# Kernel optimization log

Measured on AMD Instinct MI355X. Metric: run time of the kernel, lower is better.

Reference implementation:

```python
import jax, jax.numpy as jnp
import numpy as np

B, C, H, W = 4, 128, 128, 128
_PARAM_IDS = ["1", "2", "4", "5", "7", "8", "9", "10", "12", "13", "15", "16"]


def setup_inputs() -> dict:
    key = jax.random.key(0)
    ks = jax.random.split(key, 2 + 2 * len(_PARAM_IDS))
    scale = 1.0 / np.sqrt(C).astype(np.float32)
    inp = {
        "x": jax.random.normal(ks[0], (B, C, H, W), jnp.float32),
        "y": jax.random.uniform(ks[1], (B, C, H, W), jnp.float32),  # edge gate in [0,1)
    }
    for i, n in enumerate(_PARAM_IDS):
        inp[f"w{n}"] = jax.random.normal(ks[2 + 2 * i], (C, C), jnp.float32) * scale
        inp[f"b{n}"] = jax.random.normal(ks[3 + 2 * i], (C,), jnp.float32) * scale
    return inp


def pw(t, w, b):
    # kernel-size-1 Conv1d: t [B,C,M] -> [B,C,M]
    return jnp.einsum('oc,bcm->bom', w, t) + b[None, :, None]


def gated_scan(seq_x, seq_y, wa, ba, wb, bb, relu_first):
    # seq_x, seq_y: [L, B, C, M]; recurrence h_k = relu(conv_a(x_k) + conv_b(h_{k-1}) * y_{k-1})
    first = jax.nn.relu(seq_x[0]) if relu_first else seq_x[0]

    def step(prev, inp):
        xi, yp = inp
        h = jax.nn.relu(pw(xi, wa, ba) + pw(prev, wb, bb) * yp)
        return h, h

    _, outs = jax.lax.scan(step, first, (seq_x[1:], seq_y[:-1]))
    return jnp.concatenate([first[None], outs], axis=0)


def reference(x, y, w1, b1, w2, b2, w4, b4, w5, b5, w7, b7, w8, b8,
              w9, b9, w10, b10, w12, b12, w13, b13, w15, b15, w16, b16):
    rows_x = jnp.transpose(x, (2, 0, 1, 3))   # [H,B,C,W]
    rows_y = jnp.transpose(y, (2, 0, 1, 3))   # [H,B,C,W]
    y_cols = jnp.transpose(y, (3, 0, 1, 2))   # [W,B,C,H]

    # south scan over height (row 0 untouched, no relu on it)
    hs_rows = gated_scan(rows_x, rows_y, w1, b1, w2, b2, relu_first=False)
    hs_cols = jnp.transpose(hs_rows, (3, 1, 2, 0))  # [W,B,C,H]
    # south-east / south-west scans over width (boundary column gets relu)
    hse = gated_scan(hs_cols, y_cols, w4, b4, w5, b5, relu_first=True)
    hsw = gated_scan(hs_cols[::-1], y_cols[::-1], w7, b7, w8, b8, relu_first=True)[::-1]

    # north scan over height (reversed; boundary row gets relu)
    hn_rows = gated_scan(rows_x[::-1], rows_y[::-1], w9, b9, w10, b10, relu_first=True)[::-1]
    hn_cols = jnp.transpose(hn_rows, (3, 1, 2, 0))  # [W,B,C,H]
    hne = gated_scan(hn_cols, y_cols, w12, b12, w13, b13, relu_first=True)
    hnw = gated_scan(hn_cols[::-1], y_cols[::-1], w15, b15, w16, b16, relu_first=True)[::-1]

    out_cols = hse + hsw + hne + hnw  # [W,B,C,H]
    return jnp.transpose(out_cols, (1, 2, 3, 0))  # [B,C,H,W]
```

## Files before the change

kernel.cpp:

```cpp
#include <hip/hip_runtime.h>

typedef unsigned int uint;
typedef unsigned short ushort;
typedef __attribute__((ext_vector_type(8))) short short8;
typedef __attribute__((ext_vector_type(4))) float f32x4;

#define NPOS 16384
#define PLANE 2097152
#define XR_OFF 0
#define GR_OFF 32768
#define HP_OFF 65536
#define OR_OFF 81920
#define LDS_PH1 81920
#define LDS_PH2 114688

__device__ __forceinline__ uint fbits(float a) { return __builtin_bit_cast(uint, a); }
__device__ __forceinline__ uint rnehi(float a) {
  const uint u = fbits(a);
  return (u + 0x7FFFu + ((u >> 16) & 1u)) & 0xFFFF0000u;
}
__device__ __forceinline__ float fhi(float a) { return __builtin_bit_cast(float, rnehi(a)); }
__device__ __forceinline__ uint packhi(float a, float b) { return (rnehi(a) >> 16) | rnehi(b); }
__device__ __forceinline__ uint packtr(float a, float b) {
  return (fbits(a) >> 16) | (fbits(b) & 0xFFFF0000u);
}
__device__ __forceinline__ float b2f(uint h16) { return __builtin_bit_cast(float, h16 << 16); }

__device__ __forceinline__ f32x4 MF(short8 a, short8 b, f32x4 c) {
  return __builtin_amdgcn_mfma_f32_16x16x32_bf16(a, b, c, 0, 0, 0);
}
__device__ __forceinline__ void fill16(const void* g, char* l) {
  __builtin_amdgcn_global_load_lds((const __attribute__((address_space(1))) void*)g,
                                   (__attribute__((address_space(3))) void*)l, 16, 0, 0);
}
__device__ __forceinline__ void split8(float4 v0, float4 v1, short8& hi, short8& lo) {
  union { short8 s; uint u[4]; } H, L;
  H.u[0] = packhi(v0.x, v0.y); H.u[1] = packhi(v0.z, v0.w);
  H.u[2] = packhi(v1.x, v1.y); H.u[3] = packhi(v1.z, v1.w);
  L.u[0] = packtr(v0.x - fhi(v0.x), v0.y - fhi(v0.y));
  L.u[1] = packtr(v0.z - fhi(v0.z), v0.w - fhi(v0.w));
  L.u[2] = packtr(v1.x - fhi(v1.x), v1.y - fhi(v1.y));
  L.u[3] = packtr(v1.z - fhi(v1.z), v1.w - fhi(v1.w));
  hi = H.s; lo = L.s;
}

#define BAR() asm volatile("s_waitcnt lgkmcnt(0)\n\ts_barrier" ::: "memory")

__global__ __launch_bounds__(256) void k_transpose(const float* __restrict__ x,
                                                   const float* __restrict__ y,
                                                   ushort* __restrict__ xhi,
                                                   ushort* __restrict__ xlo,
                                                   float* __restrict__ yt1,
                                                   float* __restrict__ yt2) {
  __shared__ float tile[128][129];
  const int isY = blockIdx.x >> 9;
  const int id = blockIdx.x & 511;
  const int b = id >> 7, h = id & 127;
  const int t = threadIdx.x, half = t >> 7, lane = t & 127;
  const float* src = (isY ? y : x) + (size_t)b * PLANE + (size_t)h * 128;
  for (int c0 = 0; c0 < 128; c0 += 2) {
    const int c = c0 + half;
    tile[c][lane] = src[(size_t)c * NPOS + lane];
  }
  __syncthreads();
  if (!isY) {
    const int wq = t >> 6, cp = t & 63;
    for (int w0 = 0; w0 < 128; w0 += 4) {
      const int w = w0 + wq;
      const float v0 = tile[2 * cp][w], v1 = tile[2 * cp + 1][w];
      const size_t e = ((size_t)(b * 128 + w) * 128 + h) * 128 + 2 * cp;
      *(uint*)(xhi + e) = packhi(v0, v1);
      *(uint*)(xlo + e) = packtr(v0 - fhi(v0), v1 - fhi(v1));
    }
  } else {
    float* d1 = yt1 + (size_t)b * PLANE + (size_t)h * 128;
    float* d2 = yt2 + ((size_t)(b * 128 + h)) * NPOS;
    for (int w0 = 0; w0 < 128; w0 += 2) {
      const int w = w0 + half;
      const float v = tile[lane][w];
      d1[(size_t)w * NPOS + lane] = v;
      d2[(size_t)w * 128 + lane] = v;
    }
  }
}

template <bool RELU0, bool REV, bool MID, bool OUT16>
__device__ __forceinline__ void scan16(
    char* lds,
    const ushort* __restrict__ xhi, const ushort* __restrict__ xlo, size_t in_base,
    const float* __restrict__ gate, size_t gate_base,
    float* __restrict__ outf, ushort* __restrict__ outhi, ushort* __restrict__ outlo,
    size_t out_base, int out_ps, int out_ls,
    const float* __restrict__ Wa, const float* __restrict__ Ba,
    const float* __restrict__ Wb, const float* __restrict__ Bb,
    int* myflag, int* pflag) {
  const int t = threadIdx.x;
  const int wv = t >> 6, l = t & 63;
  const int line = l & 15, g4 = l >> 4;

  short8 wah[2][4], wal[2][4], wbh[2][4], wbl[2][4];
#pragma unroll
  for (int tt = 0; tt < 2; ++tt)
#pragma unroll
    for (int kt = 0; kt < 4; ++kt) {
      const int row = 32 * wv + 16 * tt + line;
      const int kc = 32 * kt + 8 * g4;
      split8(*(const float4*)(Wa + row * 128 + kc), *(const float4*)(Wa + row * 128 + kc + 4),
             wah[tt][kt], wal[tt][kt]);
      split8(*(const float4*)(Wb + row * 128 + kc), *(const float4*)(Wb + row * 128 + kc + 4),
             wbh[tt][kt], wbl[tt][kt]);
    }
  f32x4 baf[2], bbf[2];
#pragma unroll
  for (int tt = 0; tt < 2; ++tt) {
    baf[tt] = *(const f32x4*)(Ba + 32 * wv + 16 * tt + 4 * g4);
    bbf[tt] = *(const f32x4*)(Bb + 32 * wv + 16 * tt + 4 * g4);
  }

  auto P = [](int p) -> int { return REV ? 127 - p : p; };

  const int sp = wv >> 1;
  const ushort* xsrc = sp ? xlo : xhi;
  const int lf = l & 15;

  auto fillX = [&](int p, int slot) {
#pragma unroll
    for (int f = 0; f < 2; ++f) {
      const int kg = 2 * (wv & 1) + f;
      const int cc = 4 * kg + (l >> 4);
      fill16(xsrc + in_base + (size_t)lf * NPOS + (size_t)p * 128 + 8 * cc,
             lds + XR_OFF + slot * 8192 + sp * 4096 + kg * 1024 + l * 16);
    }
  };
  auto fillG = [&](int p, int slot) {
#pragma unroll
    for (int f = 0; f < 2; ++f)
      fill16(gate + gate_base + (size_t)lf * NPOS + (size_t)p * 128 + 32 * wv + 16 * f + 4 * (l >> 4),
             lds + GR_OFF + slot * 8192 + wv * 2048 + f * 1024 + l * 16);
  };
  auto fillO = [&](int p, int slot) {
#pragma unroll
    for (int f = 0; f < 2; ++f)
      fill16(outf + out_base + (size_t)p * out_ps + (size_t)lf * out_ls + 32 * wv + 16 * f + 4 * (l >> 4),
             lds + OR_OFF + slot * 8192 + wv * 2048 + f * 1024 + l * 16);
  };

#pragma unroll
  for (int p = 0; p < 4; ++p) {
    fillX(P(p), p);
    if (p < 3) fillG(P(p), p);
  }
  asm volatile("s_waitcnt vmcnt(0) lgkmcnt(0)\n\ts_barrier" ::: "memory");

  {
    char* Hwr = lds + HP_OFF;
#pragma unroll
    for (int tt = 0; tt < 2; ++tt) {
      const int cw = 4 * wv + 2 * tt + (g4 >> 1);
      const int boff = (cw * 16 + line) * 16 + 8 * (g4 & 1);
      const uint2 xh = *(const uint2*)(lds + XR_OFF + boff);
      const uint2 xl = *(const uint2*)(lds + XR_OFF + 4096 + boff);
      float4 f;
      f.x = b2f(xh.x & 0xFFFFu) + b2f(xl.x & 0xFFFFu);
      f.y = b2f(xh.x >> 16) + b2f(xl.x >> 16);
      f.z = b2f(xh.y & 0xFFFFu) + b2f(xl.y & 0xFFFFu);
      f.w = b2f(xh.y >> 16) + b2f(xl.y >> 16);
      if (RELU0) {
        f.x = fmaxf(f.x, 0.f); f.y = fmaxf(f.y, 0.f);
        f.z = fmaxf(f.z, 0.f); f.w = fmaxf(f.w, 0.f);
      }
      uint2 hw, lw;
      hw.x = packhi(f.x, f.y); hw.y = packhi(f.z, f.w);
      lw.x = packtr(f.x - fhi(f.x), f.y - fhi(f.y));
      lw.y = packtr(f.z - fhi(f.z), f.w - fhi(f.w));
      *(uint2*)(Hwr + boff) = hw;
      *(uint2*)(Hwr + 4096 + boff) = lw;
      const int ci0 = 32 * wv + 16 * tt + 4 * g4;
      const size_t oe = out_base + (size_t)P(0) * out_ps + (size_t)line * out_ls + ci0;
      if (OUT16) {
        *(uint2*)(outhi + oe) = hw;
        *(uint2*)(outlo + oe) = lw;
      } else {
        *(float4*)(outf + oe) = f;
      }
    }
  }
  BAR();

#pragma unroll 1
  for (int s = 1; s < 128; ++s) {
    if (MID && s == 64) {
      while (__hip_atomic_load(pflag, __ATOMIC_RELAXED, __HIP_MEMORY_SCOPE_AGENT) == 0)
        __builtin_amdgcn_s_sleep(1);
      fillO(P(64), 0);
      fillO(P(65), 1);
      fillO(P(66), 2);
    }
    if (s <= 124) {
      fillX(P(s + 3), (s + 3) & 3);
      fillG(P(s + 2), (s + 2) & 3);
      if (MID && s >= 64) fillO(P(s + 3), (s + 3) & 3);
    }
    if (MID && s == 64)
      asm volatile("s_waitcnt vmcnt(10)" ::: "memory");

    const f32x4 z = {0.f, 0.f, 0.f, 0.f};
    f32x4 aF0 = baf[0], aF1 = baf[1], aR0 = bbf[0], aR1 = bbf[1];
    f32x4 cF0 = z, cF1 = z, cR0 = z, cR1 = z;
    const char* H = lds + HP_OFF + ((s - 1) & 1) * 8192;
    const char* X = lds + XR_OFF + (s & 3) * 8192;
    __builtin_amdgcn_s_setprio(1);
#define KT(kt, F0, F1, R0, R1)                                            \
    {                                                                     \
      const short8 hh = *(const short8*)(H + kt * 1024 + l * 16);         \
      const short8 hl = *(const short8*)(H + 4096 + kt * 1024 + l * 16);  \
      const short8 xh = *(const short8*)(X + kt * 1024 + l * 16);         \
      const short8 xl = *(const short8*)(X + 4096 + kt * 1024 + l * 16);  \
      R0 = MF(wbh[0][kt], hh, R0);                                        \
      R1 = MF(wbh[1][kt], hh, R1);                                        \
      F0 = MF(wah[0][kt], xh, F0);                                        \
      F1 = MF(wah[1][kt], xh, F1);                                        \
      R0 = MF(wbh[0][kt], hl, R0);                                        \
      R1 = MF(wbh[1][kt], hl, R1);                                        \
      F0 = MF(wah[0][kt], xl, F0);                                        \
      F1 = MF(wah[1][kt], xl, F1);                                        \
      R0 = MF(wbl[0][kt], hh, R0);                                        \
      R1 = MF(wbl[1][kt], hh, R1);                                        \
      F0 = MF(wal[0][kt], xh, F0);                                        \
      F1 = MF(wal[1][kt], xh, F1);                                        \
    }
    KT(0, aF0, aF1, aR0, aR1)
    KT(1, cF0, cF1, cR0, cR1)
    KT(2, aF0, aF1, aR0, aR1)
    KT(3, cF0, cF1, cR0, cR1)
#undef KT
    __builtin_amdgcn_s_setprio(0);
    aF0 += cF0; aF1 += cF1; aR0 += cR0; aR1 += cR1;

    const char* Grd = lds + GR_OFF + ((s - 1) & 3) * 8192 + wv * 2048;
    const char* Ord = lds + OR_OFF + (s & 3) * 8192 + wv * 2048;
    char* Hwr = lds + HP_OFF + (s & 1) * 8192;
    const f32x4 aR[2] = {aR0, aR1}, aF[2] = {aF0, aF1};
#pragma unroll
    for (int tt = 0; tt < 2; ++tt) {
      const f32x4 g = *(const f32x4*)(Grd + tt * 1024 + l * 16);
      float4 h;
      h.x = fmaxf(fmaf(aR[tt][0], g[0], aF[tt][0]), 0.f);
      h.y = fmaxf(fmaf(aR[tt][1], g[1], aF[tt][1]), 0.f);
      h.z = fmaxf(fmaf(aR[tt][2], g[2], aF[tt][2]), 0.f);
      h.w = fmaxf(fmaf(aR[tt][3], g[3], aF[tt][3]), 0.f);
      uint2 hw, lw;
      hw.x = packhi(h.x, h.y); hw.y = packhi(h.z, h.w);
      lw.x = packtr(h.x - fhi(h.x), h.y - fhi(h.y));
      lw.y = packtr(h.z - fhi(h.z), h.w - fhi(h.w));
      const int cw = 4 * wv + 2 * tt + (g4 >> 1);
      const int boff = (cw * 16 + line) * 16 + 8 * (g4 & 1);
      *(uint2*)(Hwr + boff) = hw;
      *(uint2*)(Hwr + 4096 + boff) = lw;
      const int ci0 = 32 * wv + 16 * tt + 4 * g4;
      const size_t oe = out_base + (size_t)P(s) * out_ps + (size_t)line * out_ls + ci0;
      if (OUT16) {
        *(uint2*)(outhi + oe) = hw;
        *(uint2*)(outlo + oe) = lw;
      } else {
        float4 o = h;
        if (MID && s >= 64) {
          const f32x4 ov = *(const f32x4*)(Ord + tt * 1024 + l * 16);
          o.x += ov[0]; o.y += ov[1]; o.z += ov[2]; o.w += ov[3];
        }
        *(float4*)(outf + oe) = o;
      }
    }
    if constexpr (MID) {
      if (s < 64)
        asm volatile("s_waitcnt vmcnt(14)" ::: "memory");
      else
        asm volatile("s_waitcnt vmcnt(18)" ::: "memory");
    } else if constexpr (OUT16) {
      asm volatile("s_waitcnt vmcnt(18)" ::: "memory");
    } else {
      asm volatile("s_waitcnt vmcnt(12)" ::: "memory");
    }
    BAR();
    if (MID && s == 63) {
      asm volatile("s_waitcnt vmcnt(0)" ::: "memory");
      __builtin_amdgcn_s_barrier();
      if (threadIdx.x == 0)
        __hip_atomic_store(myflag, 1, __ATOMIC_RELEASE, __HIP_MEMORY_SCOPE_AGENT);
    }
  }
}

__global__ __launch_bounds__(256, 1) void k_scan_ph1(
    const ushort* __restrict__ xhi, const ushort* __restrict__ xlo,
    const float* __restrict__ yt1,
    ushort* __restrict__ hs_hi, ushort* __restrict__ hs_lo,
    ushort* __restrict__ hn_hi, ushort* __restrict__ hn_lo,
    int* __restrict__ flags,
    const float* w1, const float* b1, const float* w2, const float* b2,
    const float* w9, const float* b9, const float* w10, const float* b10) {
  __shared__ __align__(16) char lds[LDS_PH1];
  const int id = blockIdx.x;
  if (id == 0 && threadIdx.x < 128) flags[threadIdx.x] = 0;
  const int scan = id >> 5, b = (id >> 3) & 3, wg = id & 7;
  const size_t in_base = ((size_t)(b * 128 + wg * 16)) * NPOS;
  const size_t out_base = (size_t)b * PLANE + (size_t)(wg * 16) * 128;
  if (scan == 0)
    scan16<false, false, false, true>(lds, xhi, xlo, in_base, yt1, in_base,
                                      nullptr, hs_hi, hs_lo, out_base, NPOS, 128,
                                      w1, b1, w2, b2, nullptr, nullptr);
  else
    scan16<true, true, false, true>(lds, xhi, xlo, in_base, yt1, in_base,
                                    nullptr, hn_hi, hn_lo, out_base, NPOS, 128,
                                    w9, b9, w10, b10, nullptr, nullptr);
}

__global__ __launch_bounds__(256, 1) void k_scan_ph2(
    const ushort* __restrict__ hs_hi, const ushort* __restrict__ hs_lo,
    const ushort* __restrict__ hn_hi, const ushort* __restrict__ hn_lo,
    const float* __restrict__ yt2, float* __restrict__ outA, float* __restrict__ outB,
    int* __restrict__ flags,
    const float* w4, const float* b4, const float* w5, const float* b5,
    const float* w7, const float* b7, const float* w8, const float* b8,
    const float* w12, const float* b12, const float* w13, const float* b13,
    const float* w15, const float* b15, const float* w16, const float* b16) {
  __shared__ __align__(16) char lds[LDS_PH2];
  __builtin_amdgcn_fence(__ATOMIC_ACQUIRE, "agent");
  const int id = blockIdx.x;
  const int rev = id >> 6, rest = id & 63;
  const int grp = rest >> 5, b = (rest >> 3) & 3, hg = rest & 7;
  const size_t base = ((size_t)(b * 128 + hg * 16)) * NPOS;
  const ushort* ihi = grp ? hn_hi : hs_hi;
  const ushort* ilo = grp ? hn_lo : hs_lo;
  float* o = grp ? outB : outA;
  int* myf = flags + rest * 2 + rev;
  int* pf = flags + rest * 2 + (rev ^ 1);
  const float* wa; const float* ba; const float* wb; const float* bb;
  if (grp == 0) {
    wa = rev ? w7 : w4;  ba = rev ? b7 : b4;
    wb = rev ? w8 : w5;  bb = rev ? b8 : b5;
  } else {
    wa = rev ? w15 : w12; ba = rev ? b15 : b12;
    wb = rev ? w16 : w13; bb = rev ? b16 : b13;
  }
  if (rev)
    scan16<true, true, true, false>(lds, ihi, ilo, base, yt2, base,
                                    o, nullptr, nullptr, base, 128, NPOS,
                                    wa, ba, wb, bb, myf, pf);
  else
    scan16<true, false, true, false>(lds, ihi, ilo, base, yt2, base,
                                     o, nullptr, nullptr, base, 128, NPOS,
                                     wa, ba, wb, bb, myf, pf);
}

__global__ __launch_bounds__(256) void k_final(const float* __restrict__ outA,
                                               const float* __restrict__ outB,
                                               float* __restrict__ out) {
  __shared__ float tile[128][129];
  const int b = blockIdx.x >> 7, h = blockIdx.x & 127;
  const int t = threadIdx.x, half = t >> 7, lane = t & 127;
  const float* pa = outA + ((size_t)(b * 128 + h)) * NPOS;
  const float* pb = outB + ((size_t)(b * 128 + h)) * NPOS;
  for (int w0 = 0; w0 < 128; w0 += 2) {
    const int w = w0 + half;
    tile[w][lane] = pa[(size_t)w * 128 + lane] + pb[(size_t)w * 128 + lane];
  }
  __syncthreads();
  float* dst = out + (size_t)b * PLANE + (size_t)h * 128;
  for (int c0 = 0; c0 < 128; c0 += 2) {
    const int c = c0 + half;
    dst[(size_t)c * NPOS + lane] = tile[lane][c];
  }
}

extern "C" void kernel_launch(void* const* d_in, const int* in_sizes, int n_in,
                              void* d_out, int out_size, void* d_ws, size_t ws_size,
                              hipStream_t stream) {
  const float* x = (const float*)d_in[0];
  const float* y = (const float*)d_in[1];
  const float* w1 = (const float*)d_in[2];  const float* b1 = (const float*)d_in[3];
  const float* w2 = (const float*)d_in[4];  const float* b2 = (const float*)d_in[5];
  const float* w4 = (const float*)d_in[6];  const float* b4 = (const float*)d_in[7];
  const float* w5 = (const float*)d_in[8];  const float* b5 = (const float*)d_in[9];
  const float* w7 = (const float*)d_in[10]; const float* b7 = (const float*)d_in[11];
  const float* w8 = (const float*)d_in[12]; const float* b8 = (const float*)d_in[13];
  const float* w9 = (const float*)d_in[14]; const float* b9 = (const float*)d_in[15];
  const float* w10 = (const float*)d_in[16]; const float* b10 = (const float*)d_in[17];
  const float* w12 = (const float*)d_in[18]; const float* b12 = (const float*)d_in[19];
  const float* w13 = (const float*)d_in[20]; const float* b13 = (const float*)d_in[21];
  const float* w15 = (const float*)d_in[22]; const float* b15 = (const float*)d_in[23];
  const float* w16 = (const float*)d_in[24]; const float* b16 = (const float*)d_in[25];

  if (ws_size < 167772160) return;
  char* ws = (char*)d_ws;
  ushort* xt_hi = (ushort*)ws;
  ushort* xt_lo = (ushort*)(ws + 16777216);
  float* yt1 = (float*)(ws + 33554432);
  float* yt2 = (float*)(ws + 67108864);
  ushort* hs_hi = (ushort*)(ws + 100663296);
  ushort* hs_lo = (ushort*)(ws + 117440512);
  ushort* hn_hi = (ushort*)(ws + 134217728);
  ushort* hn_lo = (ushort*)(ws + 150994944);
  float* outA = (float*)ws;
  float* outB = (float*)(ws + 33554432);
  int* flags = (int*)d_out;

  dim3 blk(256);
  k_transpose<<<1024, blk, 0, stream>>>(x, y, xt_hi, xt_lo, yt1, yt2);
  k_scan_ph1<<<64, blk, 0, stream>>>(xt_hi, xt_lo, yt1, hs_hi, hs_lo, hn_hi, hn_lo, flags,
                                     w1, b1, w2, b2, w9, b9, w10, b10);
  k_scan_ph2<<<128, blk, 0, stream>>>(hs_hi, hs_lo, hn_hi, hn_lo, yt2, outA, outB, flags,
                                      w4, b4, w5, b5, w7, b7, w8, b8,
                                      w12, b12, w13, b13, w15, b15, w16, b16);
  k_final<<<512, blk, 0, stream>>>(outA, outB, (float*)d_out);
}
```

Baseline: 403.4 us.

## Halve scan workgroups to two waves, each owning 64 output channels

The recurrent scan kernels now run with 128 threads (two wavefronts) instead of 256. Each wave computes 64 output channels instead of 32, so it keeps twice as many split-bf16 weight fragments in registers and issues twice the MFMAs per step. LDS fill loops and vmcnt waits are rescaled to match. The goal is to cut cross-wave barrier cost and LDS reads of h/x per step along the serial chain. The cost is much higher register pressure and less wave-level parallelism per CU on the latency-bound recurrence.

```diff
diff --git a/kernel.cpp b/kernel.cpp
--- a/kernel.cpp
+++ b/kernel.cpp
@@ -98,51 +98,49 @@
   const int wv = t >> 6, l = t & 63;
   const int line = l & 15, g4 = l >> 4;
 
-  short8 wah[2][4], wal[2][4], wbh[2][4], wbl[2][4];
-#pragma unroll
-  for (int tt = 0; tt < 2; ++tt)
+  short8 wah[4][4], wal[4][4], wbh[4][4], wbl[4][4];
+#pragma unroll
+  for (int tt = 0; tt < 4; ++tt)
 #pragma unroll
     for (int kt = 0; kt < 4; ++kt) {
-      const int row = 32 * wv + 16 * tt + line;
+      const int row = 64 * wv + 16 * tt + line;
       const int kc = 32 * kt + 8 * g4;
       split8(*(const float4*)(Wa + row * 128 + kc), *(const float4*)(Wa + row * 128 + kc + 4),
              wah[tt][kt], wal[tt][kt]);
       split8(*(const float4*)(Wb + row * 128 + kc), *(const float4*)(Wb + row * 128 + kc + 4),
              wbh[tt][kt], wbl[tt][kt]);
     }
-  f32x4 baf[2], bbf[2];
-#pragma unroll
-  for (int tt = 0; tt < 2; ++tt) {
-    baf[tt] = *(const f32x4*)(Ba + 32 * wv + 16 * tt + 4 * g4);
-    bbf[tt] = *(const f32x4*)(Bb + 32 * wv + 16 * tt + 4 * g4);
+  f32x4 baf[4], bbf[4];
+#pragma unroll
+  for (int tt = 0; tt < 4; ++tt) {
+    baf[tt] = *(const f32x4*)(Ba + 64 * wv + 16 * tt + 4 * g4);
+    bbf[tt] = *(const f32x4*)(Bb + 64 * wv + 16 * tt + 4 * g4);
   }
 
   auto P = [](int p) -> int { return REV ? 127 - p : p; };
 
-  const int sp = wv >> 1;
-  const ushort* xsrc = sp ? xlo : xhi;
+  const ushort* xsrc = wv ? xlo : xhi;
   const int lf = l & 15;
 
   auto fillX = [&](int p, int slot) {
 #pragma unroll
-    for (int f = 0; f < 2; ++f) {
-      const int kg = 2 * (wv & 1) + f;
-      const int cc = 4 * kg + (l >> 4);
+    for (int f = 0; f < 4; ++f) {
+      const int cc = 4 * f + (l >> 4);
       fill16(xsrc + in_base + (size_t)lf * NPOS + (size_t)p * 128 + 8 * cc,
-             lds + XR_OFF + slot * 8192 + sp * 4096 + kg * 1024 + l * 16);
+             lds + XR_OFF + slot * 8192 + wv * 4096 + f * 1024 + l * 16);
     }
   };
   auto fillG = [&](int p, int slot) {
 #pragma unroll
-    for (int f = 0; f < 2; ++f)
-      fill16(gate + gate_base + (size_t)lf * NPOS + (size_t)p * 128 + 32 * wv + 16 * f + 4 * (l >> 4),
-             lds + GR_OFF + slot * 8192 + wv * 2048 + f * 1024 + l * 16);
+    for (int f = 0; f < 4; ++f)
+      fill16(gate + gate_base + (size_t)lf * NPOS + (size_t)p * 128 + 64 * wv + 16 * f + 4 * (l >> 4),
+             lds + GR_OFF + slot * 8192 + wv * 4096 + f * 1024 + l * 16);
   };
   auto fillO = [&](int p, int slot) {
 #pragma unroll
-    for (int f = 0; f < 2; ++f)
-      fill16(outf + out_base + (size_t)p * out_ps + (size_t)lf * out_ls + 32 * wv + 16 * f + 4 * (l >> 4),
-             lds + OR_OFF + slot * 8192 + wv * 2048 + f * 1024 + l * 16);
+    for (int f = 0; f < 4; ++f)
+      fill16(outf + out_base + (size_t)p * out_ps + (size_t)lf * out_ls + 64 * wv + 16 * f + 4 * (l >> 4),
+             lds + OR_OFF + slot * 8192 + wv * 4096 + f * 1024 + l * 16);
   };
 
 #pragma unroll
@@ -155,8 +153,8 @@
   {
     char* Hwr = lds + HP_OFF;
 #pragma unroll
-    for (int tt = 0; tt < 2; ++tt) {
-      const int cw = 4 * wv + 2 * tt + (g4 >> 1);
+    for (int tt = 0; tt < 4; ++tt) {
+      const int cw = 8 * wv + 2 * tt + (g4 >> 1);
       const int boff = (cw * 16 + line) * 16 + 8 * (g4 & 1);
       const uint2 xh = *(const uint2*)(lds + XR_OFF + boff);
       const uint2 xl = *(const uint2*)(lds + XR_OFF + 4096 + boff);
@@ -175,7 +173,7 @@
       lw.y = packtr(f.z - fhi(f.z), f.w - fhi(f.w));
       *(uint2*)(Hwr + boff) = hw;
       *(uint2*)(Hwr + 4096 + boff) = lw;
-      const int ci0 = 32 * wv + 16 * tt + 4 * g4;
+      const int ci0 = 64 * wv + 16 * tt + 4 * g4;
       const size_t oe = out_base + (size_t)P(0) * out_ps + (size_t)line * out_ls + ci0;
       if (OUT16) {
         *(uint2*)(outhi + oe) = hw;
@@ -202,62 +200,62 @@
       if (MID && s >= 64) fillO(P(s + 3), (s + 3) & 3);
     }
     if (MID && s == 64)
-      asm volatile("s_waitcnt vmcnt(10)" ::: "memory");
+      asm volatile("s_waitcnt vmcnt(12)" ::: "memory");
 
     const f32x4 z = {0.f, 0.f, 0.f, 0.f};
-    f32x4 aF0 = baf[0], aF1 = baf[1], aR0 = bbf[0], aR1 = bbf[1];
-    f32x4 cF0 = z, cF1 = z, cR0 = z, cR1 = z;
+    f32x4 aF[4], cF[4], aR[4], cR[4];
+#pragma unroll
+    for (int tt = 0; tt < 4; ++tt) {
+      aF[tt] = baf[tt]; aR[tt] = bbf[tt]; cF[tt] = z; cR[tt] = z;
+    }
     const char* H = lds + HP_OFF + ((s - 1) & 1) * 8192;
     const char* X = lds + XR_OFF + (s & 3) * 8192;
     __builtin_amdgcn_s_setprio(1);
-#define KT(kt, F0, F1, R0, R1)                                            \
+#define KT(kt, F, R)                                                      \
     {                                                                     \
       const short8 hh = *(const short8*)(H + kt * 1024 + l * 16);         \
       const short8 hl = *(const short8*)(H + 4096 + kt * 1024 + l * 16);  \
       const short8 xh = *(const short8*)(X + kt * 1024 + l * 16);         \
       const short8 xl = *(const short8*)(X + 4096 + kt * 1024 + l * 16);  \
-      R0 = MF(wbh[0][kt], hh, R0);                                        \
-      R1 = MF(wbh[1][kt], hh, R1);                                        \
-      F0 = MF(wah[0][kt], xh, F0);                                        \
-      F1 = MF(wah[1][kt], xh, F1);                                        \
-      R0 = MF(wbh[0][kt], hl, R0);                                        \
-      R1 = MF(wbh[1][kt], hl, R1);                                        \
-      F0 = MF(wah[0][kt], xl, F0);                                        \
-      F1 = MF(wah[1][kt], xl, F1);                                        \
-      R0 = MF(wbl[0][kt], hh, R0);                                        \
-      R1 = MF(wbl[1][kt], hh, R1);                                        \
-      F0 = MF(wal[0][kt], xh, F0);                                        \
-      F1 = MF(wal[1][kt], xh, F1);                                        \
-    }
-    KT(0, aF0, aF1, aR0, aR1)
-    KT(1, cF0, cF1, cR0, cR1)
-    KT(2, aF0, aF1, aR0, aR1)
-    KT(3, cF0, cF1, cR0, cR1)
+      _Pragma("unroll")                                                   \
+      for (int tt = 0; tt < 4; ++tt) {                                    \
+        R[tt] = MF(wbh[tt][kt], hh, R[tt]);                               \
+        F[tt] = MF(wah[tt][kt], xh, F[tt]);                               \
+        R[tt] = MF(wbh[tt][kt], hl, R[tt]);                               \
+        F[tt] = MF(wah[tt][kt], xl, F[tt]);                               \
+        R[tt] = MF(wbl[tt][kt], hh, R[tt]);                               \
+        F[tt] = MF(wal[tt][kt], xh, F[tt]);                               \
+      }                                                                   \
+    }
+    KT(0, aF, aR)
+    KT(1, cF, cR)
+    KT(2, aF, aR)
+    KT(3, cF, cR)
 #undef KT
     __builtin_amdgcn_s_setprio(0);
-    aF0 += cF0; aF1 += cF1; aR0 += cR0; aR1 += cR1;
-
-    const char* Grd = lds + GR_OFF + ((s - 1) & 3) * 8192 + wv * 2048;
-    const char* Ord = lds + OR_OFF + (s & 3) * 8192 + wv * 2048;
+
+    const char* Grd = lds + GR_OFF + ((s - 1) & 3) * 8192 + wv * 4096;
+    const char* Ord = lds + OR_OFF + (s & 3) * 8192 + wv * 4096;
     char* Hwr = lds + HP_OFF + (s & 1) * 8192;
-    const f32x4 aR[2] = {aR0, aR1}, aF[2] = {aF0, aF1};
-#pragma unroll
-    for (int tt = 0; tt < 2; ++tt) {
+#pragma unroll
+    for (int tt = 0; tt < 4; ++tt) {
+      const f32x4 Fv = aF[tt] + cF[tt];
+      const f32x4 Rv = aR[tt] + cR[tt];
       const f32x4 g = *(const f32x4*)(Grd + tt * 1024 + l * 16);
       float4 h;
-      h.x = fmaxf(fmaf(aR[tt][0], g[0], aF[tt][0]), 0.f);
-      h.y = fmaxf(fmaf(aR[tt][1], g[1], aF[tt][1]), 0.f);
-      h.z = fmaxf(fmaf(aR[tt][2], g[2], aF[tt][2]), 0.f);
-      h.w = fmaxf(fmaf(aR[tt][3], g[3], aF[tt][3]), 0.f);
+      h.x = fmaxf(fmaf(Rv[0], g[0], Fv[0]), 0.f);
+      h.y = fmaxf(fmaf(Rv[1], g[1], Fv[1]), 0.f);
+      h.z = fmaxf(fmaf(Rv[2], g[2], Fv[2]), 0.f);
+      h.w = fmaxf(fmaf(Rv[3], g[3], Fv[3]), 0.f);
       uint2 hw, lw;
       hw.x = packhi(h.x, h.y); hw.y = packhi(h.z, h.w);
       lw.x = packtr(h.x - fhi(h.x), h.y - fhi(h.y));
       lw.y = packtr(h.z - fhi(h.z), h.w - fhi(h.w));
-      const int cw = 4 * wv + 2 * tt + (g4 >> 1);
+      const int cw = 8 * wv + 2 * tt + (g4 >> 1);
       const int boff = (cw * 16 + line) * 16 + 8 * (g4 & 1);
       *(uint2*)(Hwr + boff) = hw;
       *(uint2*)(Hwr + 4096 + boff) = lw;
-      const int ci0 = 32 * wv + 16 * tt + 4 * g4;
+      const int ci0 = 64 * wv + 16 * tt + 4 * g4;
       const size_t oe = out_base + (size_t)P(s) * out_ps + (size_t)line * out_ls + ci0;
       if (OUT16) {
         *(uint2*)(outhi + oe) = hw;
@@ -273,13 +271,13 @@
     }
     if constexpr (MID) {
       if (s < 64)
-        asm volatile("s_waitcnt vmcnt(14)" ::: "memory");
+        asm volatile("s_waitcnt vmcnt(26)" ::: "memory");
       else
-        asm volatile("s_waitcnt vmcnt(18)" ::: "memory");
+        asm volatile("s_waitcnt vmcnt(34)" ::: "memory");
     } else if constexpr (OUT16) {
-      asm volatile("s_waitcnt vmcnt(18)" ::: "memory");
+      asm volatile("s_waitcnt vmcnt(38)" ::: "memory");
     } else {
-      asm volatile("s_waitcnt vmcnt(12)" ::: "memory");
+      asm volatile("s_waitcnt vmcnt(24)" ::: "memory");
     }
     BAR();
     if (MID && s == 63) {
@@ -291,7 +289,7 @@
   }
 }
 
-__global__ __launch_bounds__(256, 1) void k_scan_ph1(
+__global__ __launch_bounds__(128, 1) void k_scan_ph1(
     const ushort* __restrict__ xhi, const ushort* __restrict__ xlo,
     const float* __restrict__ yt1,
     ushort* __restrict__ hs_hi, ushort* __restrict__ hs_lo,
@@ -301,7 +299,7 @@
     const float* w9, const float* b9, const float* w10, const float* b10) {
   __shared__ __align__(16) char lds[LDS_PH1];
   const int id = blockIdx.x;
-  if (id == 0 && threadIdx.x < 128) flags[threadIdx.x] = 0;
+  if (id == 0) flags[threadIdx.x] = 0;
   const int scan = id >> 5, b = (id >> 3) & 3, wg = id & 7;
   const size_t in_base = ((size_t)(b * 128 + wg * 16)) * NPOS;
   const size_t out_base = (size_t)b * PLANE + (size_t)(wg * 16) * 128;
@@ -315,7 +313,7 @@
                                     w9, b9, w10, b10, nullptr, nullptr);
 }
 
-__global__ __launch_bounds__(256, 1) void k_scan_ph2(
+__global__ __launch_bounds__(128, 1) void k_scan_ph2(
     const ushort* __restrict__ hs_hi, const ushort* __restrict__ hs_lo,
     const ushort* __restrict__ hn_hi, const ushort* __restrict__ hn_lo,
     const float* __restrict__ yt2, float* __restrict__ outA, float* __restrict__ outB,
@@ -405,12 +403,11 @@
   float* outB = (float*)(ws + 33554432);
   int* flags = (int*)d_out;
 
-  dim3 blk(256);
-  k_transpose<<<1024, blk, 0, stream>>>(x, y, xt_hi, xt_lo, yt1, yt2);
-  k_scan_ph1<<<64, blk, 0, stream>>>(xt_hi, xt_lo, yt1, hs_hi, hs_lo, hn_hi, hn_lo, flags,
-                                     w1, b1, w2, b2, w9, b9, w10, b10);
-  k_scan_ph2<<<128, blk, 0, stream>>>(hs_hi, hs_lo, hn_hi, hn_lo, yt2, outA, outB, flags,
-                                      w4, b4, w5, b5, w7, b7, w8, b8,
-                                      w12, b12, w13, b13, w15, b15, w16, b16);
-  k_final<<<512, blk, 0, stream>>>(outA, outB, (float*)d_out);
-}
+  k_transpose<<<1024, dim3(256), 0, stream>>>(x, y, xt_hi, xt_lo, yt1, yt2);
+  k_scan_ph1<<<64, dim3(128), 0, stream>>>(xt_hi, xt_lo, yt1, hs_hi, hs_lo, hn_hi, hn_lo,
+                                           flags, w1, b1, w2, b2, w9, b9, w10, b10);
+  k_scan_ph2<<<128, dim3(128), 0, stream>>>(hs_hi, hs_lo, hn_hi, hn_lo, yt2, outA, outB,
+                                            flags, w4, b4, w5, b5, w7, b7, w8, b8,
+                                            w12, b12, w13, b13, w15, b15, w16, b16);
+  k_final<<<512, dim3(256), 0, stream>>>(outA, outB, (float*)d_out);
+}
```

New measurement: 532.7 us. 32.0% more time.
